# Optimization experiments

Measured on AMD Instinct MI355X. Metric: run time of the kernel, lower is better.

## Reference

```python
import jax, jax.numpy as jnp
import numpy as np

N_NODES = 100000
N_EDGES = 1600000
IN_DIM, HID, OUT = 256, 128, 32


def setup_inputs() -> dict:
    key = jax.random.key(0)
    ks = jax.random.split(key, 8)
    x = jax.random.normal(ks[0], (N_NODES, IN_DIM), dtype=jnp.float32)
    edge_index = jax.random.randint(ks[1], (2, N_EDGES), 0, N_NODES, dtype=jnp.int64)
    # Glorot-ish small scale to keep activations stable
    W0 = jax.random.normal(ks[2], (IN_DIM, HID), dtype=jnp.float32) * 0.05
    W1 = jax.random.normal(ks[3], (HID, HID), dtype=jnp.float32) * 0.05
    W2 = jax.random.normal(ks[4], (HID, OUT), dtype=jnp.float32) * 0.05
    b0 = jnp.zeros((HID,), jnp.float32)
    b1 = jnp.zeros((HID,), jnp.float32)
    b2 = jnp.zeros((OUT,), jnp.float32)
    return {"x": x, "edge_index": edge_index, "W0": W0, "b0": b0,
            "W1": W1, "b1": b1, "W2": W2, "b2": b2}


def reference(x, edge_index, W0, b0, W1, b1, W2, b2):
    # PyG GCNConv: add self-loops, symmetric normalization D^-1/2 A D^-1/2,
    # messages flow src (row 0) -> dst (row 1), aggregated at dst.
    n = x.shape[0]
    src, dst = edge_index[0], edge_index[1]
    ones = jnp.ones((src.shape[0],), x.dtype)
    deg = jax.ops.segment_sum(ones, dst, num_segments=n) + 1.0  # +1 for self-loop
    dinv = jax.lax.rsqrt(deg)                                   # [N]
    edge_norm = dinv[src] * dinv[dst]                           # [E]
    self_norm = dinv * dinv                                     # [N] self-loop weight

    def gcn_conv(h, W, b):
        h = h @ W                                               # [N, D_out]
        agg = jax.ops.segment_sum(h[src] * edge_norm[:, None], dst, num_segments=n)
        return agg + h * self_norm[:, None] + b

    h = gcn_conv(x, W0, b0)
    # dropout after layers i != 0: identity in eval mode (deterministic reference)
    h = gcn_conv(h, W1, b1)
    h = gcn_conv(h, W2, b2)
    return jax.nn.log_softmax(h, axis=1)
```

## Files before the change

### kernel.cpp

```cpp
#include <hip/hip_runtime.h>
#include <hip/hip_bf16.h>
#include <type_traits>

#define N_NODES 100000
#define N_EDGES 1600000
#define SLICE_N 12500
#define CAP     64

typedef float f32x4 __attribute__((ext_vector_type(4)));
typedef _Float16 f16x8 __attribute__((ext_vector_type(8)));
typedef _Float16 f16x4 __attribute__((ext_vector_type(4)));

__global__ void wconv_all_kernel(const float* __restrict__ W0, const float* __restrict__ W1,
                                 const float* __restrict__ W2, _Float16* __restrict__ Wt0,
                                 _Float16* __restrict__ Wt1, _Float16* __restrict__ Wt2) {
    int i = blockIdx.x * 256 + threadIdx.x;
    if (i < 32768) {
        int k = i / 128, col = i % 128;
        Wt0[col * 256 + k] = (_Float16)W0[i];
    } else if (i < 49152) {
        int j = i - 32768;
        int k = j / 128, col = j % 128;
        Wt1[col * 128 + k] = (_Float16)W1[j];
    } else if (i < 53248) {
        int j = i - 49152;
        int k = j / 32, col = j % 32;
        Wt2[col * 128 + k] = (_Float16)W2[j];
    }
}

#define LOADA(st, k0)                                                          \
    do {                                                                       \
        _Pragma("unroll")                                                      \
        for (int r = 0; r < 2; ++r) {                                          \
            const AT* ap = A + (size_t)gr[r] * K + (k0) + kof;                 \
            if constexpr (AF32) {                                              \
                a32[st][r][0] = *(const f32x4*)ap;                             \
                a32[st][r][1] = *(const f32x4*)(ap + 4);                       \
            } else {                                                           \
                a16[st][r] = *(const f16x8*)ap;                                \
            }                                                                  \
        }                                                                      \
    } while (0)

#define LOADB(st, k0)                                                          \
    do {                                                                       \
        _Pragma("unroll")                                                      \
        for (int c = 0; c < FC; ++c)                                           \
            bst[st][c] = *(const f16x8*)(Bt + (size_t)(c * 16 + l15) * K + (k0) + kof); \
    } while (0)

template<int K, int M, typename AT, bool SCALE>
__device__ __forceinline__ void gemm_tile_body(const AT* __restrict__ A,
                                               const _Float16* __restrict__ Bt,
                                               const float* __restrict__ dinv,
                                               _Float16* __restrict__ C,
                                               int blk, int tid) {
    constexpr bool AF32 = std::is_same<AT, float>::value;
    constexpr int FC = M / 16;
    constexpr int NIT = K / 32;
    const int wave = tid >> 6, lane = tid & 63;
    const int row0 = blk * 128;
    const int r0 = wave * 32;
    const int l15 = lane & 15, kof = (lane >> 4) * 8;

    f32x4 acc[2][FC] = {};
    int gr[2];
    #pragma unroll
    for (int r = 0; r < 2; ++r) {
        int g = row0 + r0 + r * 16 + l15;
        gr[r] = (g < N_NODES) ? g : N_NODES - 1;
    }

    f32x4 a32[3][2][2];
    f16x8 a16[3][2];
    f16x8 bst[2][FC];

    LOADA(0, 0);
    if (NIT > 1) LOADA(1, 32);
    LOADB(0, 0);

    #pragma unroll
    for (int it = 0; it < NIT; ++it) {
        if (it + 2 < NIT) LOADA((it + 2) % 3, (it + 2) * 32);
        if (it + 1 < NIT) LOADB((it + 1) % 2, (it + 1) * 32);
        f16x8 af[2];
        #pragma unroll
        for (int r = 0; r < 2; ++r) {
            if constexpr (AF32) {
                #pragma unroll
                for (int j = 0; j < 4; ++j) {
                    af[r][j] = (_Float16)a32[it % 3][r][0][j];
                    af[r][4 + j] = (_Float16)a32[it % 3][r][1][j];
                }
            } else {
                af[r] = a16[it % 3][r];
            }
        }
        #pragma unroll
        for (int c = 0; c < FC; ++c)
            #pragma unroll
            for (int r = 0; r < 2; ++r)
                acc[r][c] = __builtin_amdgcn_mfma_f32_16x16x32_f16(af[r], bst[it % 2][c], acc[r][c], 0, 0, 0);
    }

    #pragma unroll
    for (int r = 0; r < 2; ++r) {
        #pragma unroll
        for (int j = 0; j < 4; ++j) {
            int g = row0 + r0 + r * 16 + (lane >> 4) * 4 + j;
            if (g >= N_NODES) continue;
            float s = SCALE ? dinv[g] : 1.0f;
            #pragma unroll
            for (int c = 0; c < FC; ++c)
                C[(size_t)g * M + c * 16 + l15] = (_Float16)(acc[r][c][j] * s);
        }
    }
}

template<int K, int M, typename AT>
__global__ __launch_bounds__(256) void mfma_gemm_f16(const AT* __restrict__ A,
                                                     const _Float16* __restrict__ Bt,
                                                     const float* __restrict__ dinv,
                                                     _Float16* __restrict__ C) {
    gemm_tile_body<K, M, AT, true>(A, Bt, dinv, C, blockIdx.x, threadIdx.x);
}

__global__ __launch_bounds__(256) void fused_fill_gemm0(const int* __restrict__ esrc,
                                                        const int* __restrict__ edst,
                                                        int* __restrict__ cnt,
                                                        int* __restrict__ esorted,
                                                        const float* __restrict__ x,
                                                        const _Float16* __restrict__ Wt0,
                                                        _Float16* __restrict__ h) {
    const int b = blockIdx.x;
    const int g = b / 9;
    if (b % 9 == 0) {
        gemm_tile_body<256, 128, float, false>(x, Wt0, nullptr, h, g, threadIdx.x);
        return;
    }
    const int f = b - g - 1;
    const int slice = b & 7;
    const int chunk = f >> 3;
    const int base = chunk * 2048 + threadIdx.x;
    const int lo = slice * SLICE_N, hi = lo + SLICE_N;
    #pragma unroll
    for (int i = 0; i < 8; ++i) {
        int e = base + i * 256;
        if (e < N_EDGES) {
            int d = edst[e];
            if (d >= lo && d < hi) {
                int pos = atomicAdd(&cnt[d], 1);
                if (pos < CAP) esorted[(size_t)d * CAP + pos] = esrc[e];
            }
        }
    }
}

__global__ __launch_bounds__(256) void scale_dinv_kernel(const int* __restrict__ cnt,
                                                         float* __restrict__ dinv,
                                                         f16x8* __restrict__ hs) {
    int i = blockIdx.x * 256 + threadIdx.x;
    if (i >= N_NODES * 16) return;
    int n = i >> 4;
    float dn = 1.0f / sqrtf((float)cnt[n] + 1.0f);
    if ((i & 15) == 0) dinv[n] = dn;
    f16x8 v = hs[i];
    #pragma unroll
    for (int d = 0; d < 8; ++d) v[d] = (_Float16)((float)v[d] * dn);
    hs[i] = v;
}

template<int M, int G>
__global__ __launch_bounds__(256) void gather_kernel(const int* __restrict__ cnt,
                                                     const int* __restrict__ esorted,
                                                     const float* __restrict__ dinv,
                                                     const f16x8* __restrict__ hs,
                                                     const float* __restrict__ bias,
                                                     _Float16* __restrict__ out) {
    static_assert(M == 8 * G, "layout");
    constexpr int R = M / 8;
    int gid = blockIdx.x * blockDim.x + threadIdx.x;
    int node = gid / G;
    int lane = gid % G;
    if (node >= N_NODES) return;
    int len = cnt[node]; if (len > CAP) len = CAP;
    const int* __restrict__ lst = esorted + (size_t)node * CAP;
    float dn = dinv[node];
    f16x8 hv = hs[(size_t)node * R + lane];
    float acc[8];
    #pragma unroll
    for (int d = 0; d < 8; ++d) acc[d] = (float)hv[d];
    int j = 0;
    for (; j + 8 <= len; j += 8) {
        int s[8];
        f16x8 v[8];
        #pragma unroll
        for (int k = 0; k < 8; ++k) s[k] = lst[j + k];
        #pragma unroll
        for (int k = 0; k < 8; ++k) v[k] = hs[(size_t)s[k] * R + lane];
        #pragma unroll
        for (int k = 0; k < 8; ++k)
            #pragma unroll
            for (int d = 0; d < 8; ++d) acc[d] += (float)v[k][d];
    }
    for (; j < len; ++j) {
        f16x8 v = hs[(size_t)lst[j] * R + lane];
        #pragma unroll
        for (int d = 0; d < 8; ++d) acc[d] += (float)v[d];
    }
    const float* bp = bias + lane * 8;
    f16x8 o;
    #pragma unroll
    for (int d = 0; d < 8; ++d) o[d] = (_Float16)(acc[d] * dn + bp[d]);
    *((f16x8*)out + (size_t)node * R + lane) = o;
}

__global__ __launch_bounds__(256) void gather_lsm_kernel(const int* __restrict__ cnt,
                                                         const int* __restrict__ esorted,
                                                         const float* __restrict__ dinv,
                                                         const f16x8* __restrict__ hs,
                                                         const float* __restrict__ bias,
                                                         float* __restrict__ out) {
    constexpr int R = 4;
    int gid = blockIdx.x * blockDim.x + threadIdx.x;
    int node = gid / 4;
    int lane = gid % 4;
    if (node >= N_NODES) return;
    int len = cnt[node]; if (len > CAP) len = CAP;
    const int* __restrict__ lst = esorted + (size_t)node * CAP;
    float dn = dinv[node];
    f16x8 hv = hs[(size_t)node * R + lane];
    float acc[8];
    #pragma unroll
    for (int d = 0; d < 8; ++d) acc[d] = (float)hv[d];
    int j = 0;
    for (; j + 8 <= len; j += 8) {
        int s[8];
        f16x8 v[8];
        #pragma unroll
        for (int k = 0; k < 8; ++k) s[k] = lst[j + k];
        #pragma unroll
        for (int k = 0; k < 8; ++k) v[k] = hs[(size_t)s[k] * R + lane];
        #pragma unroll
        for (int k = 0; k < 8; ++k)
            #pragma unroll
            for (int d = 0; d < 8; ++d) acc[d] += (float)v[k][d];
    }
    for (; j < len; ++j) {
        f16x8 v = hs[(size_t)lst[j] * R + lane];
        #pragma unroll
        for (int d = 0; d < 8; ++d) acc[d] += (float)v[d];
    }
    const float* bp = bias + lane * 8;
    float o[8];
    #pragma unroll
    for (int d = 0; d < 8; ++d) o[d] = acc[d] * dn + bp[d];
    float m = o[0];
    #pragma unroll
    for (int d = 1; d < 8; ++d) m = fmaxf(m, o[d]);
    m = fmaxf(m, __shfl_xor(m, 1, 4));
    m = fmaxf(m, __shfl_xor(m, 2, 4));
    float s = 0.f;
    #pragma unroll
    for (int d = 0; d < 8; ++d) s += expf(o[d] - m);
    s += __shfl_xor(s, 1, 4);
    s += __shfl_xor(s, 2, 4);
    float ls = m + logf(s);
    f32x4 r0, r1;
    #pragma unroll
    for (int d = 0; d < 4; ++d) { r0[d] = o[d] - ls; r1[d] = o[4 + d] - ls; }
    f32x4* op = (f32x4*)out + (size_t)node * 8 + lane * 2;
    op[0] = r0;
    op[1] = r1;
}

extern "C" void kernel_launch(void* const* d_in, const int* in_sizes, int n_in,
                              void* d_out, int out_size, void* d_ws, size_t ws_size,
                              hipStream_t stream) {
    const float* x  = (const float*)d_in[0];
    const int*   ei = (const int*)d_in[1];
    const float* W0 = (const float*)d_in[2];
    const float* b0 = (const float*)d_in[3];
    const float* W1 = (const float*)d_in[4];
    const float* b1 = (const float*)d_in[5];
    const float* W2 = (const float*)d_in[6];
    const float* b2 = (const float*)d_in[7];
    float* out = (float*)d_out;

    char* ws = (char*)d_ws;
    float* dinv    = (float*)(ws + 0);
    int*   cnt     = (int*)  (ws + (512 << 10));
    int*   esorted = (int*)  (ws + (1 << 20));
    _Float16* Wt0  = (_Float16*)(ws + 27262976);
    _Float16* Wt1  = (_Float16*)(ws + 27262976 + 65536);
    _Float16* Wt2  = (_Float16*)(ws + 27262976 + 98304);
    _Float16* hs     = (_Float16*)(ws + 28311552);
    _Float16* bufB16 = (_Float16*)(ws + 28311552 + 26214400);
    const int* esrc = ei;
    const int* edst = ei + N_EDGES;

    (void)hipMemsetAsync(cnt, 0, N_NODES * sizeof(int), stream);
    wconv_all_kernel<<<208, 256, 0, stream>>>(W0, W1, W2, Wt0, Wt1, Wt2);
    fused_fill_gemm0<<<782 * 9, 256, 0, stream>>>(esrc, edst, cnt, esorted, x, Wt0, hs);
    scale_dinv_kernel<<<(N_NODES * 16) / 256, 256, 0, stream>>>(cnt, dinv, (f16x8*)hs);

    const int RB128 = (N_NODES + 127) / 128;

    gather_kernel<128, 16><<<(N_NODES * 16 + 255) / 256, 256, 0, stream>>>(
        cnt, esorted, dinv, (const f16x8*)hs, b0, bufB16);

    mfma_gemm_f16<128, 128, _Float16><<<RB128, 256, 0, stream>>>(bufB16, Wt1, dinv, hs);
    gather_kernel<128, 16><<<(N_NODES * 16 + 255) / 256, 256, 0, stream>>>(
        cnt, esorted, dinv, (const f16x8*)hs, b1, bufB16);

    mfma_gemm_f16<128, 32, _Float16><<<RB128, 256, 0, stream>>>(bufB16, Wt2, dinv, hs);
    gather_lsm_kernel<<<(N_NODES * 4 + 255) / 256, 256, 0, stream>>>(
        cnt, esorted, dinv, (const f16x8*)hs, b2, out);
}
```

Before: 330.7 us.

## Fuse neighbor gather with following layer GEMM into one kernel

Each gather-aggregate step now feeds its 16-node tile directly into shared memory and runs the next layer's MFMA GEMM in the same block, writing the dinv-scaled result. This removes the intermediate fp16 buffer round trip through global memory and two kernel launches. In exchange, every block reloads the weight matrix into LDS, the GEMM tile is small (16 rows), and separate ping-pong buffers are used because input and output can no longer alias.

Result: faster. 311.0 us (-6.0%).

```diff
diff --git a/kernel.cpp b/kernel.cpp
--- a/kernel.cpp
+++ b/kernel.cpp
@@ -9,7 +9,6 @@
 
 typedef float f32x4 __attribute__((ext_vector_type(4)));
 typedef _Float16 f16x8 __attribute__((ext_vector_type(8)));
-typedef _Float16 f16x4 __attribute__((ext_vector_type(4)));
 
 __global__ void wconv_all_kernel(const float* __restrict__ W0, const float* __restrict__ W1,
                                  const float* __restrict__ W2, _Float16* __restrict__ Wt0,
@@ -118,14 +117,6 @@
     }
 }
 
-template<int K, int M, typename AT>
-__global__ __launch_bounds__(256) void mfma_gemm_f16(const AT* __restrict__ A,
-                                                     const _Float16* __restrict__ Bt,
-                                                     const float* __restrict__ dinv,
-                                                     _Float16* __restrict__ C) {
-    gemm_tile_body<K, M, AT, true>(A, Bt, dinv, C, blockIdx.x, threadIdx.x);
-}
-
 __global__ __launch_bounds__(256) void fused_fill_gemm0(const int* __restrict__ esrc,
                                                         const int* __restrict__ edst,
                                                         int* __restrict__ cnt,
@@ -171,49 +162,84 @@
     hs[i] = v;
 }
 
-template<int M, int G>
-__global__ __launch_bounds__(256) void gather_kernel(const int* __restrict__ cnt,
-                                                     const int* __restrict__ esorted,
-                                                     const float* __restrict__ dinv,
-                                                     const f16x8* __restrict__ hs,
-                                                     const float* __restrict__ bias,
-                                                     _Float16* __restrict__ out) {
-    static_assert(M == 8 * G, "layout");
-    constexpr int R = M / 8;
-    int gid = blockIdx.x * blockDim.x + threadIdx.x;
-    int node = gid / G;
-    int lane = gid % G;
-    if (node >= N_NODES) return;
-    int len = cnt[node]; if (len > CAP) len = CAP;
-    const int* __restrict__ lst = esorted + (size_t)node * CAP;
-    float dn = dinv[node];
-    f16x8 hv = hs[(size_t)node * R + lane];
-    float acc[8];
-    #pragma unroll
-    for (int d = 0; d < 8; ++d) acc[d] = (float)hv[d];
-    int j = 0;
-    for (; j + 8 <= len; j += 8) {
-        int s[8];
-        f16x8 v[8];
-        #pragma unroll
-        for (int k = 0; k < 8; ++k) s[k] = lst[j + k];
-        #pragma unroll
-        for (int k = 0; k < 8; ++k) v[k] = hs[(size_t)s[k] * R + lane];
-        #pragma unroll
-        for (int k = 0; k < 8; ++k)
-            #pragma unroll
-            for (int d = 0; d < 8; ++d) acc[d] += (float)v[k][d];
-    }
-    for (; j < len; ++j) {
-        f16x8 v = hs[(size_t)lst[j] * R + lane];
-        #pragma unroll
-        for (int d = 0; d < 8; ++d) acc[d] += (float)v[d];
-    }
-    const float* bp = bias + lane * 8;
-    f16x8 o;
-    #pragma unroll
-    for (int d = 0; d < 8; ++d) o[d] = (_Float16)(acc[d] * dn + bp[d]);
-    *((f16x8*)out + (size_t)node * R + lane) = o;
+template<int OUTC>
+__global__ __launch_bounds__(256) void gather_gemm_kernel(const int* __restrict__ cnt,
+                                                          const int* __restrict__ esorted,
+                                                          const float* __restrict__ dinv,
+                                                          const f16x8* __restrict__ hs,
+                                                          const float* __restrict__ bias,
+                                                          const _Float16* __restrict__ Wt,
+                                                          _Float16* __restrict__ outh) {
+    __shared__ _Float16 Ws[OUTC][136];
+    __shared__ _Float16 As[16][136];
+    const int tid = threadIdx.x;
+
+    #pragma unroll
+    for (int i = tid; i < OUTC * 16; i += 256) {
+        int col = i >> 4, c8 = i & 15;
+        *(f16x8*)&Ws[col][c8 * 8] = *(const f16x8*)(Wt + (size_t)col * 128 + c8 * 8);
+    }
+
+    const int n16 = tid >> 4;
+    const int lane = tid & 15;
+    const int node = blockIdx.x * 16 + n16;
+    {
+        int len = cnt[node]; if (len > CAP) len = CAP;
+        const int* __restrict__ lst = esorted + (size_t)node * CAP;
+        float dn = dinv[node];
+        f16x8 hv = hs[(size_t)node * 16 + lane];
+        float acc[8];
+        #pragma unroll
+        for (int d = 0; d < 8; ++d) acc[d] = (float)hv[d];
+        int j = 0;
+        for (; j + 8 <= len; j += 8) {
+            int s[8];
+            f16x8 v[8];
+            #pragma unroll
+            for (int k = 0; k < 8; ++k) s[k] = lst[j + k];
+            #pragma unroll
+            for (int k = 0; k < 8; ++k) v[k] = hs[(size_t)s[k] * 16 + lane];
+            #pragma unroll
+            for (int k = 0; k < 8; ++k)
+                #pragma unroll
+                for (int d = 0; d < 8; ++d) acc[d] += (float)v[k][d];
+        }
+        for (; j < len; ++j) {
+            f16x8 v = hs[(size_t)lst[j] * 16 + lane];
+            #pragma unroll
+            for (int d = 0; d < 8; ++d) acc[d] += (float)v[d];
+        }
+        const float* bp = bias + lane * 8;
+        f16x8 o;
+        #pragma unroll
+        for (int d = 0; d < 8; ++d) o[d] = (_Float16)(acc[d] * dn + bp[d]);
+        *(f16x8*)&As[n16][lane * 8] = o;
+    }
+    __syncthreads();
+
+    const int wave = tid >> 6, l64 = tid & 63;
+    const int l15 = l64 & 15, kq = l64 >> 4;
+    constexpr int NF = OUTC / 16;
+    constexpr int FPW = (NF + 3) / 4;
+    #pragma unroll
+    for (int f = 0; f < FPW; ++f) {
+        int cf = wave * FPW + f;
+        if (cf < NF) {
+            int col = cf * 16 + l15;
+            f32x4 a2 = {};
+            #pragma unroll
+            for (int it = 0; it < 4; ++it) {
+                f16x8 af = *(const f16x8*)&As[l15][it * 32 + kq * 8];
+                f16x8 bf = *(const f16x8*)&Ws[col][it * 32 + kq * 8];
+                a2 = __builtin_amdgcn_mfma_f32_16x16x32_f16(af, bf, a2, 0, 0, 0);
+            }
+            #pragma unroll
+            for (int j = 0; j < 4; ++j) {
+                int g = blockIdx.x * 16 + kq * 4 + j;
+                outh[(size_t)g * OUTC + col] = (_Float16)(a2[j] * dinv[g]);
+            }
+        }
+    }
 }
 
 __global__ __launch_bounds__(256) void gather_lsm_kernel(const int* __restrict__ cnt,
@@ -295,8 +321,9 @@
     _Float16* Wt0  = (_Float16*)(ws + 27262976);
     _Float16* Wt1  = (_Float16*)(ws + 27262976 + 65536);
     _Float16* Wt2  = (_Float16*)(ws + 27262976 + 98304);
-    _Float16* hs     = (_Float16*)(ws + 28311552);
-    _Float16* bufB16 = (_Float16*)(ws + 28311552 + 26214400);
+    _Float16* hs   = (_Float16*)(ws + 28311552);
+    _Float16* hs1  = (_Float16*)(ws + 28311552 + 26214400);
+    _Float16* hs2  = (_Float16*)(ws + 28311552 + 52428800);
     const int* esrc = ei;
     const int* edst = ei + N_EDGES;
 
@@ -305,16 +332,12 @@
     fused_fill_gemm0<<<782 * 9, 256, 0, stream>>>(esrc, edst, cnt, esorted, x, Wt0, hs);
     scale_dinv_kernel<<<(N_NODES * 16) / 256, 256, 0, stream>>>(cnt, dinv, (f16x8*)hs);
 
-    const int RB128 = (N_NODES + 127) / 128;
-
-    gather_kernel<128, 16><<<(N_NODES * 16 + 255) / 256, 256, 0, stream>>>(
-        cnt, esorted, dinv, (const f16x8*)hs, b0, bufB16);
-
-    mfma_gemm_f16<128, 128, _Float16><<<RB128, 256, 0, stream>>>(bufB16, Wt1, dinv, hs);
-    gather_kernel<128, 16><<<(N_NODES * 16 + 255) / 256, 256, 0, stream>>>(
-        cnt, esorted, dinv, (const f16x8*)hs, b1, bufB16);
-
-    mfma_gemm_f16<128, 32, _Float16><<<RB128, 256, 0, stream>>>(bufB16, Wt2, dinv, hs);
+    gather_gemm_kernel<128><<<N_NODES / 16, 256, 0, stream>>>(
+        cnt, esorted, dinv, (const f16x8*)hs, b0, Wt1, hs1);
+
+    gather_gemm_kernel<32><<<N_NODES / 16, 256, 0, stream>>>(
+        cnt, esorted, dinv, (const f16x8*)hs1, b1, Wt2, hs2);
+
     gather_lsm_kernel<<<(N_NODES * 4 + 255) / 256, 256, 0, stream>>>(
-        cnt, esorted, dinv, (const f16x8*)hs, b2, out);
-}
+        cnt, esorted, dinv, (const f16x8*)hs2, b2, out);
+}
```
